# Kernel tuning notes

Hardware: AMD Instinct MI355X
Metric: run time of the kernel (lower is better)

The kernel has to match this reference:

```python
import jax, jax.numpy as jnp
import numpy as np

NUM_HEADS = 16
HEAD_DIM = 64


def setup_inputs() -> dict:
    key = jax.random.key(0)
    k1, k2, k3 = jax.random.split(key, 3)
    B, N, D = 4, 2048, NUM_HEADS * HEAD_DIM
    q = jax.random.normal(k1, (B, N, D), dtype=jnp.float32)
    k = jax.random.normal(k2, (B, N, D), dtype=jnp.float32)
    v = jax.random.normal(k3, (B, N, D), dtype=jnp.float32)
    # causal mask: True where attention is allowed
    attn_mask = jnp.tril(jnp.ones((N, N), dtype=bool))
    return {"q": q, "k": k, "v": v, "attn_mask": attn_mask}


def reference(q, k, v, attn_mask):
    B, N, D = q.shape
    H, Hd = NUM_HEADS, HEAD_DIM
    # [B, N, H*Hd] -> [B, H, N, Hd]
    qh = q.reshape(B, N, H, Hd).transpose(0, 2, 1, 3)
    kh = k.reshape(B, N, H, Hd).transpose(0, 2, 1, 3)
    vh = v.reshape(B, N, H, Hd).transpose(0, 2, 1, 3)
    scale = 1.0 / jnp.sqrt(jnp.asarray(Hd, dtype=q.dtype))
    scores = jnp.einsum('bhqd,bhkd->bhqk', qh, kh) * scale  # [B,H,N,N]
    scores = jnp.where(attn_mask[None, None, :, :], scores, -jnp.inf)
    probs = jax.nn.softmax(scores, axis=-1)
    y = jnp.einsum('bhqk,bhkd->bhqd', probs, vh)  # [B,H,N,Hd]
    return y.transpose(0, 2, 1, 3).reshape(B, N, H * Hd)
```

## Files before the change

### kernel.cpp

```cpp
#include <hip/hip_runtime.h>

#define RS 1024
#define SEQLEN 2048

typedef __fp16 f16;
typedef __attribute__((ext_vector_type(2))) __fp16 half2v;
typedef __attribute__((ext_vector_type(4))) __fp16 half4v;
typedef __attribute__((ext_vector_type(8))) __fp16 half8v;
typedef __attribute__((ext_vector_type(4))) float float4v;

__device__ __forceinline__ half8v pack8h(float4v a, float4v b) {
  union { half8v v; half2v h[4]; } u;
  u.h[0] = __builtin_amdgcn_cvt_pkrtz(a[0], a[1]);
  u.h[1] = __builtin_amdgcn_cvt_pkrtz(a[2], a[3]);
  u.h[2] = __builtin_amdgcn_cvt_pkrtz(b[0], b[1]);
  u.h[3] = __builtin_amdgcn_cvt_pkrtz(b[2], b[3]);
  return u.v;
}

template<bool DOMASK>
__device__ __forceinline__ void compute_tile(
    const f16* __restrict__ Klds, const f16* __restrict__ VB,
    const half8v (&aq)[2], float4v (&o)[4], float& lp,
    int quad, int lm, int wlm)
{
  float4v sfr[4];
  #pragma unroll
  for (int nb = 0; nb < 4; ++nb) sfr[nb] = (float4v){0.f, 0.f, 0.f, 0.f};

  __builtin_amdgcn_s_setprio(1);
  #pragma unroll
  for (int nb = 0; nb < 4; ++nb) {
    const int row = nb*16 + lm;
    #pragma unroll
    for (int s = 0; s < 2; ++s) {
      const half8v ak = *(const half8v*)&Klds[row*64 + (((s*4 + quad) ^ (lm & 7)) * 8)];
      sfr[nb] = __builtin_amdgcn_mfma_f32_16x16x32_f16(ak, aq[s], sfr[nb], 0, 0, 0);
    }
  }
  __builtin_amdgcn_s_setprio(0);

  half4v pa[4];
  float acc = 0.f;
  #pragma unroll
  for (int nb = 0; nb < 4; ++nb) {
    float p[4];
    #pragma unroll
    for (int r = 0; r < 4; ++r) {
      const int n = nb*16 + quad*4 + r;
      const float e = __builtin_amdgcn_exp2f(sfr[nb][r]);
      p[r] = (DOMASK && (n > wlm)) ? 0.f : e;
    }
    acc += (p[0] + p[1]) + (p[2] + p[3]);
    union { half4v v; half2v h[2]; } u;
    u.h[0] = __builtin_amdgcn_cvt_pkrtz(p[0], p[1]);
    u.h[1] = __builtin_amdgcn_cvt_pkrtz(p[2], p[3]);
    pa[nb] = u.v;
  }
  lp += acc;

  __builtin_amdgcn_s_setprio(1);
  #pragma unroll
  for (int e = 0; e < 2; ++e) {
    #pragma unroll
    for (int nb = 0; nb < 4; ++nb) {
      const int kvq = nb*4 + quad;
      union { half8v v; half4v h[2]; } uu;
      uu.v = *(const half8v*)&VB[kvq*256 + (((e*16 + lm) ^ kvq) * 8)];
      o[2*e]     = __builtin_amdgcn_mfma_f32_16x16x16f16(pa[nb], uu.h[0], o[2*e],     0, 0, 0);
      o[2*e + 1] = __builtin_amdgcn_mfma_f32_16x16x16f16(pa[nb], uu.h[1], o[2*e + 1], 0, 0, 0);
    }
  }
  __builtin_amdgcn_s_setprio(0);
}

__global__ __launch_bounds__(512, 4) void fa_fwd(
    const float* __restrict__ Qg, const float* __restrict__ Kg,
    const float* __restrict__ Vg, float* __restrict__ Og)
{
  __shared__ __align__(16) f16 Klds[2][64*64];
  __shared__ __align__(16) f16 VB[2][64*64];

  const int tid  = threadIdx.x;
  const int w    = tid >> 6;
  const int lane = tid & 63;
  const int quad = lane >> 4;
  const int lm   = lane & 15;
  const int wlm  = (w & 3)*16 + lm;

  const int bid = blockIdx.x;
  const int bh  = bid & 63;
  const int g   = (bid >> 6) & 3;
  const int s   = bid >> 8;
  const int st  = (s == 0) ? 15 - g : (s == 1) ? 8 + g : (s == 2) ? 7 - g : g;
  const int j1  = 2*st + 1;
  const int j1w = 2*st + (w >> 2);

  const size_t headoff = (size_t)(bh >> 4) * SEQLEN * RS + (size_t)(bh & 15) * 64;
  const float* Kb = Kg + headoff;
  const float* Vb = Vg + headoff;

  const float qs = 0.18033688011112042f;
  half8v aq[2];
  {
    const float* qp = Qg + headoff + (size_t)(st*128 + w*16 + lm) * RS + quad*8;
    aq[0] = pack8h(*(const float4v*)qp * qs,        *(const float4v*)(qp + 4) * qs);
    aq[1] = pack8h(*(const float4v*)(qp + 32) * qs, *(const float4v*)(qp + 36) * qs);
  }

  float4v o[4] = {};
  float lp = 0.f;

  const bool doK = (tid >= 256);
  const int kr   = tid & 255;
  const int krow = kr >> 3, kcb = kr & 7;
  const int rgrp = kr >> 4, dgrp = kr & 15;
  const int ve   = dgrp >> 3;
  const int vv   = (dgrp >> 2) & 1;
  const int lmb  = (dgrp & 3) * 4;

  float4v pr[4];
  auto loadKV = [&](int kv0) {
    if (doK) {
      const float* kp = Kb + (size_t)(kv0 + krow) * RS + kcb*8;
      pr[0] = *(const float4v*)kp;       pr[1] = *(const float4v*)(kp + 4);
      const float* kp2 = kp + (size_t)32 * RS;
      pr[2] = *(const float4v*)kp2;      pr[3] = *(const float4v*)(kp2 + 4);
    } else {
      const float* vp = Vb + (size_t)(kv0 + rgrp*4) * RS + dgrp*4;
      pr[0] = *(const float4v*)vp;
      pr[1] = *(const float4v*)(vp + RS);
      pr[2] = *(const float4v*)(vp + 2*RS);
      pr[3] = *(const float4v*)(vp + 3*RS);
    }
  };
  auto stageKV = [&](f16* Kd, f16* Vd) {
    if (doK) {
      *(half8v*)&Kd[krow*64 + ((kcb ^ (krow & 7)) * 8)] = pack8h(pr[0], pr[1]);
      const int row2 = krow + 32;
      *(half8v*)&Kd[row2*64 + ((kcb ^ (row2 & 7)) * 8)] = pack8h(pr[2], pr[3]);
    } else {
      #pragma unroll
      for (int cc = 0; cc < 4; ++cc) {
        union { half4v v; half2v h[2]; } u;
        u.h[0] = __builtin_amdgcn_cvt_pkrtz(pr[0][cc], pr[1][cc]);
        u.h[1] = __builtin_amdgcn_cvt_pkrtz(pr[2][cc], pr[3][cc]);
        const int lmv = lmb + cc;
        *(half4v*)&Vd[rgrp*256 + (((ve*16 + lmv) ^ rgrp) * 8) + vv*4] = u.v;
      }
    }
  };

  loadKV(0);
  stageKV(Klds[0], VB[0]);
  loadKV(64);
  __syncthreads();

  for (int j = 0; j <= j1; ++j) {
    const int cur = j & 1;
    if (j < j1) {
      stageKV(Klds[cur ^ 1], VB[cur ^ 1]);
      if (j + 1 < j1) loadKV((j + 2) * 64);
    }
    if (j <= j1w) {
      if (j < j1w)
        compute_tile<false>(Klds[cur], VB[cur], aq, o, lp, quad, lm, wlm);
      else
        compute_tile<true >(Klds[cur], VB[cur], aq, o, lp, quad, lm, wlm);
    }
    __syncthreads();
  }

  float l = lp;
  l += __shfl_xor(l, 16);
  l += __shfl_xor(l, 32);
  const float linv = 1.0f / l;
  #pragma unroll
  for (int r = 0; r < 4; ++r) {
    const float nrm = __shfl(linv, quad*4 + r);
    float* op = Og + headoff + (size_t)(st*128 + w*16 + quad*4 + r) * RS;
    #pragma unroll
    for (int db = 0; db < 4; ++db)
      op[db*16 + lm] = o[db][r] * nrm;
  }
}

extern "C" void kernel_launch(void* const* d_in, const int* in_sizes, int n_in,
                              void* d_out, int out_size, void* d_ws, size_t ws_size,
                              hipStream_t stream) {
  const float* q = (const float*)d_in[0];
  const float* k = (const float*)d_in[1];
  const float* v = (const float*)d_in[2];
  float* out = (float*)d_out;
  fa_fwd<<<dim3(16 * 64), dim3(512), 0, stream>>>(q, k, v, out);
}
```

Baseline: 178.8 us.

## Halve block to 4 waves, each computing two 16-row query tiles

The block shrinks from 8 to 4 waves, and each wave now owns 32 query rows handled as two 16-row sub-tiles. Every K and V fragment read from LDS therefore feeds two MFMAs, which halves LDS reads per FLOP. Since there are no longer separate K and V loader waves, every thread loads and stages both K and V, split across the compute phase to overlap global loads with math. The cost is more registers per thread and fewer waves per block for hiding latency.

```diff
diff --git a/kernel.cpp b/kernel.cpp
--- a/kernel.cpp
+++ b/kernel.cpp
@@ -21,12 +21,14 @@
 template<bool DOMASK>
 __device__ __forceinline__ void compute_tile(
     const f16* __restrict__ Klds, const f16* __restrict__ VB,
-    const half8v (&aq)[2], float4v (&o)[4], float& lp,
-    int quad, int lm, int wlm)
+    const half8v (&aq)[2][2], float4v (&o)[2][4], float (&lp)[2],
+    int quad, int lm, int wlm0)
 {
-  float4v sfr[4];
-  #pragma unroll
-  for (int nb = 0; nb < 4; ++nb) sfr[nb] = (float4v){0.f, 0.f, 0.f, 0.f};
+  float4v sfr[2][4];
+  #pragma unroll
+  for (int a = 0; a < 2; ++a)
+    #pragma unroll
+    for (int nb = 0; nb < 4; ++nb) sfr[a][nb] = (float4v){0.f, 0.f, 0.f, 0.f};
 
   __builtin_amdgcn_s_setprio(1);
   #pragma unroll
@@ -35,29 +37,34 @@
     #pragma unroll
     for (int s = 0; s < 2; ++s) {
       const half8v ak = *(const half8v*)&Klds[row*64 + (((s*4 + quad) ^ (lm & 7)) * 8)];
-      sfr[nb] = __builtin_amdgcn_mfma_f32_16x16x32_f16(ak, aq[s], sfr[nb], 0, 0, 0);
+      sfr[0][nb] = __builtin_amdgcn_mfma_f32_16x16x32_f16(ak, aq[0][s], sfr[0][nb], 0, 0, 0);
+      sfr[1][nb] = __builtin_amdgcn_mfma_f32_16x16x32_f16(ak, aq[1][s], sfr[1][nb], 0, 0, 0);
     }
   }
   __builtin_amdgcn_s_setprio(0);
 
-  half4v pa[4];
-  float acc = 0.f;
-  #pragma unroll
-  for (int nb = 0; nb < 4; ++nb) {
-    float p[4];
-    #pragma unroll
-    for (int r = 0; r < 4; ++r) {
-      const int n = nb*16 + quad*4 + r;
-      const float e = __builtin_amdgcn_exp2f(sfr[nb][r]);
-      p[r] = (DOMASK && (n > wlm)) ? 0.f : e;
-    }
-    acc += (p[0] + p[1]) + (p[2] + p[3]);
-    union { half4v v; half2v h[2]; } u;
-    u.h[0] = __builtin_amdgcn_cvt_pkrtz(p[0], p[1]);
-    u.h[1] = __builtin_amdgcn_cvt_pkrtz(p[2], p[3]);
-    pa[nb] = u.v;
-  }
-  lp += acc;
+  half4v pa[2][4];
+  #pragma unroll
+  for (int a = 0; a < 2; ++a) {
+    const int wlm = wlm0 + a*16;
+    float acc = 0.f;
+    #pragma unroll
+    for (int nb = 0; nb < 4; ++nb) {
+      float p[4];
+      #pragma unroll
+      for (int r = 0; r < 4; ++r) {
+        const int n = nb*16 + quad*4 + r;
+        const float e = __builtin_amdgcn_exp2f(sfr[a][nb][r]);
+        p[r] = (DOMASK && (n > wlm)) ? 0.f : e;
+      }
+      acc += (p[0] + p[1]) + (p[2] + p[3]);
+      union { half4v v; half2v h[2]; } u;
+      u.h[0] = __builtin_amdgcn_cvt_pkrtz(p[0], p[1]);
+      u.h[1] = __builtin_amdgcn_cvt_pkrtz(p[2], p[3]);
+      pa[a][nb] = u.v;
+    }
+    lp[a] += acc;
+  }
 
   __builtin_amdgcn_s_setprio(1);
   #pragma unroll
@@ -67,14 +74,16 @@
       const int kvq = nb*4 + quad;
       union { half8v v; half4v h[2]; } uu;
       uu.v = *(const half8v*)&VB[kvq*256 + (((e*16 + lm) ^ kvq) * 8)];
-      o[2*e]     = __builtin_amdgcn_mfma_f32_16x16x16f16(pa[nb], uu.h[0], o[2*e],     0, 0, 0);
-      o[2*e + 1] = __builtin_amdgcn_mfma_f32_16x16x16f16(pa[nb], uu.h[1], o[2*e + 1], 0, 0, 0);
+      o[0][2*e]     = __builtin_amdgcn_mfma_f32_16x16x16f16(pa[0][nb], uu.h[0], o[0][2*e],     0, 0, 0);
+      o[0][2*e + 1] = __builtin_amdgcn_mfma_f32_16x16x16f16(pa[0][nb], uu.h[1], o[0][2*e + 1], 0, 0, 0);
+      o[1][2*e]     = __builtin_amdgcn_mfma_f32_16x16x16f16(pa[1][nb], uu.h[0], o[1][2*e],     0, 0, 0);
+      o[1][2*e + 1] = __builtin_amdgcn_mfma_f32_16x16x16f16(pa[1][nb], uu.h[1], o[1][2*e + 1], 0, 0, 0);
     }
   }
   __builtin_amdgcn_s_setprio(0);
 }
 
-__global__ __launch_bounds__(512, 4) void fa_fwd(
+__global__ __launch_bounds__(256, 4) void fa_fwd(
     const float* __restrict__ Qg, const float* __restrict__ Kg,
     const float* __restrict__ Vg, float* __restrict__ Og)
 {
@@ -86,7 +95,7 @@
   const int lane = tid & 63;
   const int quad = lane >> 4;
   const int lm   = lane & 15;
-  const int wlm  = (w & 3)*16 + lm;
+  const int wlm0 = (w & 1)*32 + lm;
 
   const int bid = blockIdx.x;
   const int bh  = bid & 63;
@@ -94,94 +103,98 @@
   const int s   = bid >> 8;
   const int st  = (s == 0) ? 15 - g : (s == 1) ? 8 + g : (s == 2) ? 7 - g : g;
   const int j1  = 2*st + 1;
-  const int j1w = 2*st + (w >> 2);
+  const int j1w = 2*st + (w >> 1);
 
   const size_t headoff = (size_t)(bh >> 4) * SEQLEN * RS + (size_t)(bh & 15) * 64;
   const float* Kb = Kg + headoff;
   const float* Vb = Vg + headoff;
 
   const float qs = 0.18033688011112042f;
-  half8v aq[2];
-  {
-    const float* qp = Qg + headoff + (size_t)(st*128 + w*16 + lm) * RS + quad*8;
-    aq[0] = pack8h(*(const float4v*)qp * qs,        *(const float4v*)(qp + 4) * qs);
-    aq[1] = pack8h(*(const float4v*)(qp + 32) * qs, *(const float4v*)(qp + 36) * qs);
-  }
-
-  float4v o[4] = {};
-  float lp = 0.f;
-
-  const bool doK = (tid >= 256);
-  const int kr   = tid & 255;
-  const int krow = kr >> 3, kcb = kr & 7;
-  const int rgrp = kr >> 4, dgrp = kr & 15;
+  half8v aq[2][2];
+  #pragma unroll
+  for (int a = 0; a < 2; ++a) {
+    const float* qp = Qg + headoff + (size_t)(st*128 + w*32 + a*16 + lm) * RS + quad*8;
+    aq[a][0] = pack8h(*(const float4v*)qp * qs,        *(const float4v*)(qp + 4) * qs);
+    aq[a][1] = pack8h(*(const float4v*)(qp + 32) * qs, *(const float4v*)(qp + 36) * qs);
+  }
+
+  float4v o[2][4] = {};
+  float lp[2] = {0.f, 0.f};
+
+  const int krow = tid >> 3, kcb = tid & 7;
+  const int rgrp = tid >> 4, dgrp = tid & 15;
   const int ve   = dgrp >> 3;
   const int vv   = (dgrp >> 2) & 1;
   const int lmb  = (dgrp & 3) * 4;
 
-  float4v pr[4];
-  auto loadKV = [&](int kv0) {
-    if (doK) {
-      const float* kp = Kb + (size_t)(kv0 + krow) * RS + kcb*8;
-      pr[0] = *(const float4v*)kp;       pr[1] = *(const float4v*)(kp + 4);
-      const float* kp2 = kp + (size_t)32 * RS;
-      pr[2] = *(const float4v*)kp2;      pr[3] = *(const float4v*)(kp2 + 4);
-    } else {
-      const float* vp = Vb + (size_t)(kv0 + rgrp*4) * RS + dgrp*4;
-      pr[0] = *(const float4v*)vp;
-      pr[1] = *(const float4v*)(vp + RS);
-      pr[2] = *(const float4v*)(vp + 2*RS);
-      pr[3] = *(const float4v*)(vp + 3*RS);
-    }
-  };
-  auto stageKV = [&](f16* Kd, f16* Vd) {
-    if (doK) {
-      *(half8v*)&Kd[krow*64 + ((kcb ^ (krow & 7)) * 8)] = pack8h(pr[0], pr[1]);
-      const int row2 = krow + 32;
-      *(half8v*)&Kd[row2*64 + ((kcb ^ (row2 & 7)) * 8)] = pack8h(pr[2], pr[3]);
-    } else {
-      #pragma unroll
-      for (int cc = 0; cc < 4; ++cc) {
-        union { half4v v; half2v h[2]; } u;
-        u.h[0] = __builtin_amdgcn_cvt_pkrtz(pr[0][cc], pr[1][cc]);
-        u.h[1] = __builtin_amdgcn_cvt_pkrtz(pr[2][cc], pr[3][cc]);
-        const int lmv = lmb + cc;
-        *(half4v*)&Vd[rgrp*256 + (((ve*16 + lmv) ^ rgrp) * 8) + vv*4] = u.v;
-      }
-    }
-  };
-
-  loadKV(0);
-  stageKV(Klds[0], VB[0]);
-  loadKV(64);
+  float4v pk[4], pv[4];
+  auto loadK = [&](int kv0) {
+    const float* kp = Kb + (size_t)(kv0 + krow) * RS + kcb*8;
+    pk[0] = *(const float4v*)kp;       pk[1] = *(const float4v*)(kp + 4);
+    const float* kp2 = kp + (size_t)32 * RS;
+    pk[2] = *(const float4v*)kp2;      pk[3] = *(const float4v*)(kp2 + 4);
+  };
+  auto loadV = [&](int kv0) {
+    const float* vp = Vb + (size_t)(kv0 + rgrp*4) * RS + dgrp*4;
+    pv[0] = *(const float4v*)vp;
+    pv[1] = *(const float4v*)(vp + RS);
+    pv[2] = *(const float4v*)(vp + 2*RS);
+    pv[3] = *(const float4v*)(vp + 3*RS);
+  };
+  auto stageK = [&](f16* Kd) {
+    *(half8v*)&Kd[krow*64 + ((kcb ^ (krow & 7)) * 8)] = pack8h(pk[0], pk[1]);
+    const int row2 = krow + 32;
+    *(half8v*)&Kd[row2*64 + ((kcb ^ (row2 & 7)) * 8)] = pack8h(pk[2], pk[3]);
+  };
+  auto stageV = [&](f16* Vd) {
+    #pragma unroll
+    for (int cc = 0; cc < 4; ++cc) {
+      union { half4v v; half2v h[2]; } u;
+      u.h[0] = __builtin_amdgcn_cvt_pkrtz(pv[0][cc], pv[1][cc]);
+      u.h[1] = __builtin_amdgcn_cvt_pkrtz(pv[2][cc], pv[3][cc]);
+      const int lmv = lmb + cc;
+      *(half4v*)&Vd[rgrp*256 + (((ve*16 + lmv) ^ rgrp) * 8) + vv*4] = u.v;
+    }
+  };
+
+  loadK(0); loadV(0);
+  stageK(Klds[0]); stageV(VB[0]);
+  loadK(64);
   __syncthreads();
 
   for (int j = 0; j <= j1; ++j) {
     const int cur = j & 1;
     if (j < j1) {
-      stageKV(Klds[cur ^ 1], VB[cur ^ 1]);
-      if (j + 1 < j1) loadKV((j + 2) * 64);
+      stageK(Klds[cur ^ 1]);
+      loadV((j + 1) * 64);
     }
     if (j <= j1w) {
       if (j < j1w)
-        compute_tile<false>(Klds[cur], VB[cur], aq, o, lp, quad, lm, wlm);
+        compute_tile<false>(Klds[cur], VB[cur], aq, o, lp, quad, lm, wlm0);
       else
-        compute_tile<true >(Klds[cur], VB[cur], aq, o, lp, quad, lm, wlm);
+        compute_tile<true >(Klds[cur], VB[cur], aq, o, lp, quad, lm, wlm0);
+    }
+    if (j < j1) {
+      stageV(VB[cur ^ 1]);
+      if (j + 1 < j1) loadK((j + 2) * 64);
     }
     __syncthreads();
   }
 
-  float l = lp;
-  l += __shfl_xor(l, 16);
-  l += __shfl_xor(l, 32);
-  const float linv = 1.0f / l;
-  #pragma unroll
-  for (int r = 0; r < 4; ++r) {
-    const float nrm = __shfl(linv, quad*4 + r);
-    float* op = Og + headoff + (size_t)(st*128 + w*16 + quad*4 + r) * RS;
-    #pragma unroll
-    for (int db = 0; db < 4; ++db)
-      op[db*16 + lm] = o[db][r] * nrm;
+  #pragma unroll
+  for (int a = 0; a < 2; ++a) {
+    float l = lp[a];
+    l += __shfl_xor(l, 16);
+    l += __shfl_xor(l, 32);
+    const float linv = 1.0f / l;
+    #pragma unroll
+    for (int r = 0; r < 4; ++r) {
+      const float nrm = __shfl(linv, quad*4 + r);
+      float* op = Og + headoff + (size_t)(st*128 + w*32 + a*16 + quad*4 + r) * RS;
+      #pragma unroll
+      for (int db = 0; db < 4; ++db)
+        op[db*16 + lm] = o[a][db][r] * nrm;
+    }
   }
 }
 
@@ -192,5 +205,5 @@
   const float* k = (const float*)d_in[1];
   const float* v = (const float*)d_in[2];
   float* out = (float*)d_out;
-  fa_fwd<<<dim3(16 * 64), dim3(512), 0, stream>>>(q, k, v, out);
-}
+  fa_fwd<<<dim3(16 * 64), dim3(256), 0, stream>>>(q, k, v, out);
+}
```

Result: slower. 279.1 us (+56.0%).
